# Kernel optimization log

Measured on AMD Instinct MI355X. Metric: run time of the kernel, lower is better.

## Reference

```python
import jax, jax.numpy as jnp
import numpy as np

NUM_EMBEDDINGS = 512
EMBEDDING_DIM = 128

def setup_inputs() -> dict:
    key = jax.random.key(0)
    k1, k2 = jax.random.split(key)
    z_e = jax.random.normal(k1, (32, EMBEDDING_DIM, 64, 64), dtype=jnp.float32)
    embedding = jax.random.normal(k2, (NUM_EMBEDDINGS, EMBEDDING_DIM), dtype=jnp.float32)
    return {"z_e": z_e, "embedding": embedding}

def reference(z_e, embedding):
    B, C, H, W = z_e.shape
    # (B,C,H,W) -> (N, C) with N = B*H*W
    z_flat = jnp.transpose(z_e, (0, 2, 3, 1)).reshape(-1, C)
    # squared L2 distance via expansion: ||z||^2 - 2 z.E^T + ||E||^2  (avoids (N,K,C) intermediate)
    z_sq = jnp.sum(z_flat * z_flat, axis=-1, keepdims=True)          # (N,1)
    e_sq = jnp.sum(embedding * embedding, axis=-1)                    # (K,)
    dist = z_sq - 2.0 * jnp.einsum('nc,kc->nk', z_flat, embedding) + e_sq  # (N,K)
    indices = jnp.argmin(dist, axis=1)                                # (N,)
    z_q = embedding[indices].reshape(B, H, W, C)                      # gather
    return jnp.transpose(z_q, (0, 3, 1, 2))                           # (B,C,H,W)
```

## Files before the change

### kernel.cpp

```cpp
#include <hip/hip_runtime.h>
#include <float.h>

#define NUM_EMB 512
#define DIM     128
#define HWX     4096
#define NPOS    (32 * 4096)
#define MARGIN  0.35f
#define FULLPAD 0.01f

#define WS_PAIR  ((size_t)0)
#define WS_E16   ((size_t)33554432)
#define WS_ESQ   ((size_t)33685504)
#define WS_WL    ((size_t)34211840)
#define WS_CNT   ((size_t)34736128)
#define WS_NEED  ((size_t)34736384)

using half8 = __attribute__((ext_vector_type(8))) _Float16;
using f32x4 = __attribute__((ext_vector_type(4))) float;

__global__ void prep_kernel(const float* __restrict__ emb, _Float16* __restrict__ e16,
                            float* __restrict__ esq, int* __restrict__ cnt) {
    int k = blockIdx.x * blockDim.x + threadIdx.x;
    if (k == 0) { cnt[0] = 0; cnt[1] = 0; }
    if (k < NUM_EMB) {
        const float4* row = (const float4*)(emb + (size_t)k * DIM);
        _Float16* dst = e16 + (size_t)k * DIM;
        float s0 = 0.f, s1 = 0.f, s2 = 0.f, s3 = 0.f;
        #pragma unroll
        for (int c = 0; c < DIM / 4; ++c) {
            float4 v = row[c];
            s0 = fmaf(v.x, v.x, s0);
            s1 = fmaf(v.y, v.y, s1);
            s2 = fmaf(v.z, v.z, s2);
            s3 = fmaf(v.w, v.w, s3);
            dst[4 * c + 0] = (_Float16)v.x;
            dst[4 * c + 1] = (_Float16)v.y;
            dst[4 * c + 2] = (_Float16)v.z;
            dst[4 * c + 3] = (_Float16)v.w;
        }
        esq[k] = (s0 + s1) + (s2 + s3);
    }
}

__global__ __launch_bounds__(256) void gemm_argmin(const float* __restrict__ z,
                                                   const _Float16* __restrict__ e16,
                                                   const float* __restrict__ esq,
                                                   const float* __restrict__ emb,
                                                   float* __restrict__ out,
                                                   int* __restrict__ wl,
                                                   int* __restrict__ wp,
                                                   int* __restrict__ cnt) {
    __shared__ __align__(16) char Ash[128 * 272];
    __shared__ float mB1[2][128];
    __shared__ float mB2[2][128];
    __shared__ float mB3[2][128];
    __shared__ int   ish[128];

    int t = threadIdx.x;
    int lane = t & 63, wave = t >> 6;
    int wm = wave & 1, wn = wave >> 1;
    int quad = lane >> 4, l15 = lane & 15;
    int n0 = blockIdx.x * 128;
    int bb = n0 >> 12;
    int hw0 = n0 & 4095;

    {
        int g = t & 31, cq = t >> 5;
        int hw = hw0 + 4 * g;
        const float* zp = z + (size_t)bb * DIM * HWX + (size_t)cq * 16 * HWX + hw;
        char* arow0 = Ash + (4 * g) * 272;
        int xr = g & 7;
        #pragma unroll
        for (int k = 0; k < 2; ++k) {
            float4 v[8];
            #pragma unroll
            for (int c = 0; c < 8; ++c)
                v[c] = *(const float4*)(zp + (size_t)(k * 8 + c) * HWX);
            int slotb = ((2 * cq + k) ^ xr) * 16;
            #pragma unroll
            for (int j = 0; j < 4; ++j) {
                half8 hv;
                #pragma unroll
                for (int c = 0; c < 8; ++c) {
                    float f = (j == 0) ? v[c].x : (j == 1) ? v[c].y
                            : (j == 2) ? v[c].z : v[c].w;
                    hv[c] = (_Float16)f;
                }
                *(half8*)(arow0 + j * 272 + slotb) = hv;
            }
        }
    }
    __syncthreads();

    float b1[16], b2[16], b3[16];
    #pragma unroll
    for (int s = 0; s < 16; ++s) { b1[s] = 3.0e38f; b2[s] = 3.0e38f; b3[s] = 3.0e38f; }

    const char* abase = Ash + (wm * 64 + l15) * 272 + (quad ^ (l15 >> 2)) * 16;
    const char* ebase = (const char*)e16 + ((size_t)(wn * 32 + l15) << 8) + quad * 16;
    const float* eqb  = esq + wn * 32 + l15;

    for (int tile = 0; tile < 8; ++tile) {
        half8 bf[2][4];
        {
            const char* eb = ebase + (size_t)tile * 64 * 256;
            #pragma unroll
            for (int nt = 0; nt < 2; ++nt)
                #pragma unroll
                for (int kc = 0; kc < 4; ++kc)
                    bf[nt][kc] = *(const half8*)(eb + nt * 4096 + kc * 64);
        }
        float es0 = eqb[tile * 64];
        float es1 = eqb[tile * 64 + 16];

        f32x4 acc[4][2];
        #pragma unroll
        for (int mt = 0; mt < 4; ++mt)
            #pragma unroll
            for (int nt = 0; nt < 2; ++nt)
                acc[mt][nt] = (f32x4){0.f, 0.f, 0.f, 0.f};

        #pragma unroll
        for (int kc = 0; kc < 4; ++kc) {
            half8 af[4];
            #pragma unroll
            for (int mt = 0; mt < 4; ++mt)
                af[mt] = *(const half8*)(abase + mt * (16 * 272) + ((kc ^ (mt & 1)) * 64));
            #pragma unroll
            for (int mt = 0; mt < 4; ++mt)
                #pragma unroll
                for (int nt = 0; nt < 2; ++nt)
                    acc[mt][nt] = __builtin_amdgcn_mfma_f32_16x16x32_f16(af[mt], bf[nt][kc], acc[mt][nt], 0, 0, 0);
        }

        #pragma unroll
        for (int nt = 0; nt < 2; ++nt) {
            unsigned code = (unsigned)(tile * 64 + wn * 32 + nt * 16 + l15);
            float es = nt ? es1 : es0;
            #pragma unroll
            for (int mt = 0; mt < 4; ++mt)
                #pragma unroll
                for (int r = 0; r < 4; ++r) {
                    int s = mt * 4 + r;
                    float sc = fmaf(-2.0f, acc[mt][nt][r], es);
                    float p = __uint_as_float((__float_as_uint(sc) & 0xFFFFFE00u) | code);
                    float t1 = fmaxf(b1[s], p);
                    b1[s] = fminf(b1[s], p);
                    float t2 = fmaxf(b2[s], t1);
                    b2[s] = fminf(b2[s], t1);
                    b3[s] = fminf(b3[s], t2);
                }
        }
    }

    #pragma unroll
    for (int d = 1; d < 16; d <<= 1) {
        #pragma unroll
        for (int s = 0; s < 16; ++s) {
            float o1 = __shfl_xor(b1[s], d, 64);
            float o2 = __shfl_xor(b2[s], d, 64);
            float o3 = __shfl_xor(b3[s], d, 64);
            float u1 = fmaxf(b1[s], o1);
            b1[s] = fminf(b1[s], o1);
            float l2 = fminf(b2[s], o2);
            float w  = fmaxf(u1, l2);
            b2[s] = fminf(u1, l2);
            b3[s] = fminf(fminf(b3[s], o3), w);
        }
    }
    if (l15 == 0) {
        #pragma unroll
        for (int s = 0; s < 16; ++s) {
            int m = wm * 64 + (s >> 2) * 16 + quad * 4 + (s & 3);
            mB1[wn][m] = b1[s];
            mB2[wn][m] = b2[s];
            mB3[wn][m] = b3[s];
        }
    }
    __syncthreads();
    if (t < 128) {
        float a1 = mB1[0][t], c1 = mB1[1][t];
        float a2 = mB2[0][t], c2 = mB2[1][t];
        float a3 = mB3[0][t], c3 = mB3[1][t];
        float u1 = fmaxf(a1, c1);
        float m1 = fminf(a1, c1);
        float l2 = fminf(a2, c2);
        float m2 = fminf(u1, l2);
        float m3 = fminf(fminf(a3, c3), fmaxf(u1, l2));
        int ix1 = (int)(__float_as_uint(m1) & 511u);
        ish[t] = ix1;
        if (m3 - m1 < MARGIN + FULLPAD) {
            int p = atomicAdd(cnt, 1);
            wl[p] = n0 + t;
        } else if (m2 - m1 < MARGIN) {
            int p = atomicAdd(cnt + 1, 1);
            int ix2 = (int)(__float_as_uint(m2) & 511u);
            wp[2 * p]     = n0 + t;
            wp[2 * p + 1] = (ix1 << 9) | ix2;
        }
    }
    __syncthreads();

    {
        int g = t & 31, cq = t >> 5;
        int hw = hw0 + 4 * g;
        int i0 = ish[4 * g + 0], i1v = ish[4 * g + 1];
        int i2 = ish[4 * g + 2], i3 = ish[4 * g + 3];
        const float4* e0 = (const float4*)(emb + (size_t)i0 * DIM) + cq * 4;
        const float4* e1 = (const float4*)(emb + (size_t)i1v * DIM) + cq * 4;
        const float4* e2 = (const float4*)(emb + (size_t)i2 * DIM) + cq * 4;
        const float4* e3 = (const float4*)(emb + (size_t)i3 * DIM) + cq * 4;
        float* ob = out + (size_t)bb * DIM * HWX + (size_t)cq * 16 * HWX + hw;
        #pragma unroll
        for (int cc = 0; cc < 4; ++cc) {
            float4 r0 = e0[cc], r1 = e1[cc], r2 = e2[cc], r3 = e3[cc];
            *(float4*)(ob + (size_t)(4 * cc + 0) * HWX) = (float4){r0.x, r1.x, r2.x, r3.x};
            *(float4*)(ob + (size_t)(4 * cc + 1) * HWX) = (float4){r0.y, r1.y, r2.y, r3.y};
            *(float4*)(ob + (size_t)(4 * cc + 2) * HWX) = (float4){r0.z, r1.z, r2.z, r3.z};
            *(float4*)(ob + (size_t)(4 * cc + 3) * HWX) = (float4){r0.w, r1.w, r2.w, r3.w};
        }
    }
}

__global__ __launch_bounds__(256) void pair_kernel(const float* __restrict__ z,
                                                   const float* __restrict__ emb,
                                                   const float* __restrict__ esq,
                                                   const int* __restrict__ wp,
                                                   const int* __restrict__ cnt,
                                                   float* __restrict__ out) {
    int cp = cnt[1];
    int t = threadIdx.x;
    int l16 = t & 15;
    int gid = blockIdx.x * 16 + (t >> 4);
    for (int e = gid; e < cp; e += gridDim.x * 16) {
        int n  = wp[2 * e];
        int ii = wp[2 * e + 1];
        int i1 = (ii >> 9) & 511, i2 = ii & 511;
        int b = n >> 12, hw = n & 4095;
        const float* zp = z + (size_t)b * DIM * HWX + hw;
        const float* e1 = emb + (size_t)i1 * DIM;
        const float* e2 = emb + (size_t)i2 * DIM;
        float zv[8];
        #pragma unroll
        for (int j = 0; j < 8; ++j)
            zv[j] = zp[(size_t)(l16 * 8 + j) * HWX];
        float d1 = 0.f, d2 = 0.f;
        #pragma unroll
        for (int j = 0; j < 8; ++j) {
            d1 = fmaf(zv[j], e1[l16 * 8 + j], d1);
            d2 = fmaf(zv[j], e2[l16 * 8 + j], d2);
        }
        #pragma unroll
        for (int d = 1; d < 16; d <<= 1) {
            d1 += __shfl_xor(d1, d, 16);
            d2 += __shfl_xor(d2, d, 16);
        }
        float s1 = fmaf(-2.f, d1, esq[i1]);
        float s2 = fmaf(-2.f, d2, esq[i2]);
        bool take2 = (s2 < s1) || (s2 == s1 && i2 < i1);
        int win = take2 ? i2 : i1;
        const float* er = emb + (size_t)win * DIM;
        float* ob = out + (size_t)b * DIM * HWX + hw;
        #pragma unroll
        for (int j = 0; j < 8; ++j)
            ob[(size_t)(l16 * 8 + j) * HWX] = er[l16 * 8 + j];
    }
}

__global__ __launch_bounds__(256) void refine_kernel(const float* __restrict__ z,
                                                     const float* __restrict__ emb,
                                                     const float* __restrict__ esq,
                                                     const int* __restrict__ wl,
                                                     const int* __restrict__ cnt,
                                                     float* __restrict__ out) {
    __shared__ __align__(16) float zsh[16][132];
    __shared__ __align__(16) float esh[64][132];
    __shared__ float rs[16][16];
    __shared__ int   ri[16][16];
    __shared__ int   nsh[16];
    __shared__ int   ksh[16];

    int t = threadIdx.x;
    int te = t & 15, tc = t >> 4;
    int count = *cnt;

    for (int base = blockIdx.x * 16; base < count; base += 256 * 16) {
        {
            int e = t >> 4, d = t & 15;
            int ge = base + e;
            if (ge > count - 1) ge = count - 1;
            int n = wl[ge];
            if (d == 0) nsh[e] = n;
            int b = n >> 12, hw = n & 4095;
            const float* zp = z + (size_t)b * DIM * HWX + hw;
            #pragma unroll
            for (int jj = 0; jj < 8; ++jj)
                zsh[e][d + 16 * jj] = zp[(size_t)(d + 16 * jj) * HWX];
        }

        float bs = 3.0e38f; int bk = 0;

        for (int tile = 0; tile < 8; ++tile) {
            __syncthreads();
            {
                const float4* gsrc = (const float4*)(emb + (size_t)tile * 64 * DIM);
                #pragma unroll
                for (int jj = 0; jj < 8; ++jj) {
                    int f = jj * 256 + t;
                    int k = f >> 5, q = f & 31;
                    float4 v = gsrc[f];
                    *(float4*)&esh[k][q * 4] = v;
                }
                if (t < 64) esh[t][128] = esq[tile * 64 + t];
            }
            __syncthreads();

            float acc[4] = {0.f, 0.f, 0.f, 0.f};
            #pragma unroll 4
            for (int c4 = 0; c4 < 32; ++c4) {
                float4 zv = *(const float4*)&zsh[te][c4 * 4];
                #pragma unroll
                for (int j = 0; j < 4; ++j) {
                    float4 ev = *(const float4*)&esh[tc * 4 + j][c4 * 4];
                    acc[j] = fmaf(zv.x, ev.x, acc[j]);
                    acc[j] = fmaf(zv.y, ev.y, acc[j]);
                    acc[j] = fmaf(zv.z, ev.z, acc[j]);
                    acc[j] = fmaf(zv.w, ev.w, acc[j]);
                }
            }
            #pragma unroll
            for (int j = 0; j < 4; ++j) {
                int k = tile * 64 + tc * 4 + j;
                float es = esh[tc * 4 + j][128];
                float s = fmaf(-2.f, acc[j], es);
                if (s < bs) { bs = s; bk = k; }
            }
        }
        __syncthreads();
        rs[te][tc] = bs; ri[te][tc] = bk;
        __syncthreads();
        if (t < 16) {
            float s = rs[t][0]; int k = ri[t][0];
            #pragma unroll
            for (int q = 1; q < 16; ++q) {
                float s2 = rs[t][q]; int k2 = ri[t][q];
                bool take = (s2 < s) || (s2 == s && k2 < k);
                s = take ? s2 : s;
                k = take ? k2 : k;
            }
            ksh[t] = k;
        }
        __syncthreads();
        {
            int e = t >> 4, d = t & 15;
            int n = nsh[e];
            int b = n >> 12, hw = n & 4095;
            int kk = ksh[e];
            const float* er = emb + (size_t)kk * DIM;
            float* ob = out + (size_t)b * DIM * HWX + hw;
            #pragma unroll
            for (int jj = 0; jj < 8; ++jj)
                ob[(size_t)(d + 16 * jj) * HWX] = er[d + 16 * jj];
        }
        __syncthreads();
    }
}

__global__ void esq_kernel(const float* __restrict__ emb, float* __restrict__ e_sq) {
    int k = blockIdx.x * blockDim.x + threadIdx.x;
    if (k < NUM_EMB) {
        const float4* row = (const float4*)(emb + k * DIM);
        float s0 = 0.f, s1 = 0.f, s2 = 0.f, s3 = 0.f;
        #pragma unroll
        for (int c = 0; c < DIM / 4; ++c) {
            float4 v = row[c];
            s0 = fmaf(v.x, v.x, s0); s1 = fmaf(v.y, v.y, s1);
            s2 = fmaf(v.z, v.z, s2); s3 = fmaf(v.w, v.w, s3);
        }
        e_sq[k] = (s0 + s1) + (s2 + s3);
    }
}

__global__ __launch_bounds__(256) void vq_kernel(const float* __restrict__ z,
                                                 const float* __restrict__ emb,
                                                 const float* __restrict__ e_sq,
                                                 float* __restrict__ out) {
    int n = blockIdx.x * 256 + threadIdx.x;
    int b = n >> 12, hw = n & 4095;
    const float* zb = z + (size_t)b * DIM * HWX + hw;
    float zr[DIM];
    #pragma unroll
    for (int c = 0; c < DIM; ++c) zr[c] = zb[(size_t)c * HWX];
    float best = FLT_MAX; int besti = 0;
    for (int k = 0; k < NUM_EMB; ++k) {
        const float4* er = (const float4*)(emb + k * DIM);
        float d0 = 0.f, d1 = 0.f, d2 = 0.f, d3 = 0.f;
        #pragma unroll
        for (int c = 0; c < DIM / 4; ++c) {
            float4 e = er[c];
            d0 = fmaf(zr[4 * c + 0], e.x, d0);
            d1 = fmaf(zr[4 * c + 1], e.y, d1);
            d2 = fmaf(zr[4 * c + 2], e.z, d2);
            d3 = fmaf(zr[4 * c + 3], e.w, d3);
        }
        float s = e_sq[k] - 2.f * ((d0 + d1) + (d2 + d3));
        if (s < best) { best = s; besti = k; }
    }
    float* ob = out + (size_t)b * DIM * HWX + hw;
    const float4* sel = (const float4*)(emb + (size_t)besti * DIM);
    #pragma unroll
    for (int c4 = 0; c4 < DIM / 4; ++c4) {
        float4 v = sel[c4];
        ob[(size_t)(4 * c4 + 0) * HWX] = v.x;
        ob[(size_t)(4 * c4 + 1) * HWX] = v.y;
        ob[(size_t)(4 * c4 + 2) * HWX] = v.z;
        ob[(size_t)(4 * c4 + 3) * HWX] = v.w;
    }
}

extern "C" void kernel_launch(void* const* d_in, const int* in_sizes, int n_in,
                              void* d_out, int out_size, void* d_ws, size_t ws_size,
                              hipStream_t stream) {
    const float* z   = (const float*)d_in[0];
    const float* emb = (const float*)d_in[1];
    float* out = (float*)d_out;

    if (ws_size < WS_NEED) {
        float* e_sq = (float*)d_ws;
        esq_kernel<<<(NUM_EMB + 255) / 256, 256, 0, stream>>>(emb, e_sq);
        vq_kernel<<<NPOS / 256, 256, 0, stream>>>(z, emb, e_sq, out);
        return;
    }

    char* ws = (char*)d_ws;
    _Float16* e16 = (_Float16*)(ws + WS_E16);
    float*    esq = (float*)(ws + WS_ESQ);
    int*      wl  = (int*)(ws + WS_WL);
    int*      wp  = (int*)(ws + WS_PAIR);
    int*      cnt = (int*)(ws + WS_CNT);

    prep_kernel<<<2, 256, 0, stream>>>(emb, e16, esq, cnt);
    gemm_argmin<<<NPOS / 128, 256, 0, stream>>>(z, e16, esq, emb, out, wl, wp, cnt);
    pair_kernel<<<1024, 256, 0, stream>>>(z, emb, esq, wp, cnt, out);
    refine_kernel<<<256, 256, 0, stream>>>(z, emb, esq, wl, cnt, out);
}
```

Before: 229.6 us.

## Fuse top-2 fp32 re-check into GEMM kernel, drop separate pair kernel

Instead of pushing ambiguous top-2 positions to a worklist and re-checking them in a separate pair kernel, every position in the GEMM block now recomputes exact fp32 distances to its two best candidates. It reads the z tile again and splits the partial dot products across threads through shared memory before choosing the winner and writing the output. This removes a kernel launch, the pair worklist, and the scattered rewrite of output rows. In exchange it does extra fp32 work and z reads for all positions, not only the ambiguous ones. The refine kernel grid is also doubled to 512 blocks, with its stride now taken from gridDim.

```diff
diff --git a/kernel.cpp b/kernel.cpp
--- a/kernel.cpp
+++ b/kernel.cpp
@@ -8,7 +8,6 @@
 #define MARGIN  0.35f
 #define FULLPAD 0.01f
 
-#define WS_PAIR  ((size_t)0)
 #define WS_E16   ((size_t)33554432)
 #define WS_ESQ   ((size_t)33685504)
 #define WS_WL    ((size_t)34211840)
@@ -48,7 +47,6 @@
                                                    const float* __restrict__ emb,
                                                    float* __restrict__ out,
                                                    int* __restrict__ wl,
-                                                   int* __restrict__ wp,
                                                    int* __restrict__ cnt) {
     __shared__ __align__(16) char Ash[128 * 272];
     __shared__ float mB1[2][128];
@@ -188,16 +186,68 @@
         float m2 = fminf(u1, l2);
         float m3 = fminf(fminf(a3, c3), fmaxf(u1, l2));
         int ix1 = (int)(__float_as_uint(m1) & 511u);
-        ish[t] = ix1;
+        int ix2 = (int)(__float_as_uint(m2) & 511u);
+        ish[t] = ix1 | (ix2 << 9);
         if (m3 - m1 < MARGIN + FULLPAD) {
             int p = atomicAdd(cnt, 1);
             wl[p] = n0 + t;
-        } else if (m2 - m1 < MARGIN) {
-            int p = atomicAdd(cnt + 1, 1);
-            int ix2 = (int)(__float_as_uint(m2) & 511u);
-            wp[2 * p]     = n0 + t;
-            wp[2 * p + 1] = (ix1 << 9) | ix2;
-        }
+        }
+    }
+    __syncthreads();
+
+    {
+        int g = t & 31, cq = t >> 5;
+        int hw = hw0 + 4 * g;
+        const float* zp = z + (size_t)bb * DIM * HWX + (size_t)cq * 16 * HWX + hw;
+        int ii[4];
+        #pragma unroll
+        for (int j = 0; j < 4; ++j) ii[j] = ish[4 * g + j];
+        float d1[4] = {0.f, 0.f, 0.f, 0.f};
+        float d2[4] = {0.f, 0.f, 0.f, 0.f};
+        #pragma unroll
+        for (int k = 0; k < 2; ++k) {
+            float4 v[8];
+            #pragma unroll
+            for (int c = 0; c < 8; ++c)
+                v[c] = *(const float4*)(zp + (size_t)(k * 8 + c) * HWX);
+            #pragma unroll
+            for (int j = 0; j < 4; ++j) {
+                const float* e1p = emb + (size_t)(ii[j] & 511) * DIM + cq * 16 + k * 8;
+                const float* e2p = emb + (size_t)((ii[j] >> 9) & 511) * DIM + cq * 16 + k * 8;
+                float4 p0 = *(const float4*)(e1p), p1 = *(const float4*)(e1p + 4);
+                float4 q0 = *(const float4*)(e2p), q1 = *(const float4*)(e2p + 4);
+                float e1c[8] = {p0.x, p0.y, p0.z, p0.w, p1.x, p1.y, p1.z, p1.w};
+                float e2c[8] = {q0.x, q0.y, q0.z, q0.w, q1.x, q1.y, q1.z, q1.w};
+                #pragma unroll
+                for (int c = 0; c < 8; ++c) {
+                    float zc = (j == 0) ? v[c].x : (j == 1) ? v[c].y
+                             : (j == 2) ? v[c].z : v[c].w;
+                    d1[j] = fmaf(zc, e1c[c], d1[j]);
+                    d2[j] = fmaf(zc, e2c[c], d2[j]);
+                }
+            }
+        }
+        float2* part = (float2*)Ash;
+        #pragma unroll
+        for (int j = 0; j < 4; ++j)
+            part[(4 * g + j) * 9 + cq] = make_float2(d1[j], d2[j]);
+    }
+    __syncthreads();
+    if (t < 128) {
+        int ii = ish[t];
+        int i1 = ii & 511, i2 = (ii >> 9) & 511;
+        const float2* pr = (const float2*)Ash + (size_t)t * 9;
+        float d1 = 0.f, d2 = 0.f;
+        #pragma unroll
+        for (int cq = 0; cq < 8; ++cq) {
+            float2 pv = pr[cq];
+            d1 += pv.x;
+            d2 += pv.y;
+        }
+        float s1 = fmaf(-2.f, d1, esq[i1]);
+        float s2 = fmaf(-2.f, d2, esq[i2]);
+        bool take2 = (s2 < s1) || (s2 == s1 && i2 < i1);
+        ish[t] = take2 ? i2 : i1;
     }
     __syncthreads();
 
@@ -219,51 +269,6 @@
             *(float4*)(ob + (size_t)(4 * cc + 2) * HWX) = (float4){r0.z, r1.z, r2.z, r3.z};
             *(float4*)(ob + (size_t)(4 * cc + 3) * HWX) = (float4){r0.w, r1.w, r2.w, r3.w};
         }
-    }
-}
-
-__global__ __launch_bounds__(256) void pair_kernel(const float* __restrict__ z,
-                                                   const float* __restrict__ emb,
-                                                   const float* __restrict__ esq,
-                                                   const int* __restrict__ wp,
-                                                   const int* __restrict__ cnt,
-                                                   float* __restrict__ out) {
-    int cp = cnt[1];
-    int t = threadIdx.x;
-    int l16 = t & 15;
-    int gid = blockIdx.x * 16 + (t >> 4);
-    for (int e = gid; e < cp; e += gridDim.x * 16) {
-        int n  = wp[2 * e];
-        int ii = wp[2 * e + 1];
-        int i1 = (ii >> 9) & 511, i2 = ii & 511;
-        int b = n >> 12, hw = n & 4095;
-        const float* zp = z + (size_t)b * DIM * HWX + hw;
-        const float* e1 = emb + (size_t)i1 * DIM;
-        const float* e2 = emb + (size_t)i2 * DIM;
-        float zv[8];
-        #pragma unroll
-        for (int j = 0; j < 8; ++j)
-            zv[j] = zp[(size_t)(l16 * 8 + j) * HWX];
-        float d1 = 0.f, d2 = 0.f;
-        #pragma unroll
-        for (int j = 0; j < 8; ++j) {
-            d1 = fmaf(zv[j], e1[l16 * 8 + j], d1);
-            d2 = fmaf(zv[j], e2[l16 * 8 + j], d2);
-        }
-        #pragma unroll
-        for (int d = 1; d < 16; d <<= 1) {
-            d1 += __shfl_xor(d1, d, 16);
-            d2 += __shfl_xor(d2, d, 16);
-        }
-        float s1 = fmaf(-2.f, d1, esq[i1]);
-        float s2 = fmaf(-2.f, d2, esq[i2]);
-        bool take2 = (s2 < s1) || (s2 == s1 && i2 < i1);
-        int win = take2 ? i2 : i1;
-        const float* er = emb + (size_t)win * DIM;
-        float* ob = out + (size_t)b * DIM * HWX + hw;
-        #pragma unroll
-        for (int j = 0; j < 8; ++j)
-            ob[(size_t)(l16 * 8 + j) * HWX] = er[l16 * 8 + j];
     }
 }
 
@@ -284,7 +289,7 @@
     int te = t & 15, tc = t >> 4;
     int count = *cnt;
 
-    for (int base = blockIdx.x * 16; base < count; base += 256 * 16) {
+    for (int base = blockIdx.x * 16; base < count; base += gridDim.x * 16) {
         {
             int e = t >> 4, d = t & 15;
             int ge = base + e;
@@ -436,11 +441,9 @@
     _Float16* e16 = (_Float16*)(ws + WS_E16);
     float*    esq = (float*)(ws + WS_ESQ);
     int*      wl  = (int*)(ws + WS_WL);
-    int*      wp  = (int*)(ws + WS_PAIR);
     int*      cnt = (int*)(ws + WS_CNT);
 
     prep_kernel<<<2, 256, 0, stream>>>(emb, e16, esq, cnt);
-    gemm_argmin<<<NPOS / 128, 256, 0, stream>>>(z, e16, esq, emb, out, wl, wp, cnt);
-    pair_kernel<<<1024, 256, 0, stream>>>(z, emb, esq, wp, cnt, out);
-    refine_kernel<<<256, 256, 0, stream>>>(z, emb, esq, wl, cnt, out);
-}
+    gemm_argmin<<<NPOS / 128, 256, 0, stream>>>(z, e16, esq, emb, out, wl, cnt);
+    refine_kernel<<<512, 256, 0, stream>>>(z, emb, esq, wl, cnt, out);
+}
```

Measured after the change: 214.2 us. -6.7%, faster.
